# Performance work log

Hardware: AMD Instinct MI355X
Metric: run time of the kernel (lower is better)

The kernel has to match this reference:

```python
import jax, jax.numpy as jnp
import numpy as np

N_LEVELS = 8
N_FEATS = 8            # features per level
BASE_RES = 16
PER_LEVEL_SCALE = 1.2599210739135742
LOG2_HASHMAP = 19
TABLE_PAD = 8192       # padded per-level table rows (>= max level size 6568)
N_POINTS = 262144


def _level_params(l):
    # tcnn: scale = base * s^l - 1 ; res = ceil(scale)+1 ; size = min(2^19, round_up(res^2, 8))
    scale = BASE_RES * (PER_LEVEL_SCALE ** l) - 1.0
    res = int(np.ceil(scale)) + 1
    size = min(1 << LOG2_HASHMAP, ((res * res + 7) // 8) * 8)
    return float(scale), res, size


def hashgrid_encode(x, table):
    """x: [N,2] in [0,1), table: [L, TABLE_PAD, F]. Returns [N, L*F]."""
    outs = []
    for l in range(N_LEVELS):
        scale, res, size = _level_params(l)
        pos = x * jnp.float32(scale) + jnp.float32(0.5)
        pg = jnp.floor(pos)
        frac = pos - pg
        pg = pg.astype(jnp.int32)
        # Smoothstep interpolation weights: t^2 (3 - 2t)
        w = frac * frac * (3.0 - 2.0 * frac)          # [N,2]
        feat = jnp.zeros((x.shape[0], N_FEATS), dtype=table.dtype)
        for dx in (0, 1):
            wx = w[:, 0] if dx else 1.0 - w[:, 0]
            for dy in (0, 1):
                wy = w[:, 1] if dy else 1.0 - w[:, 1]
                # dense grid index (all levels here fit the hashmap), modulo level size as in tcnn
                idx = ((pg[:, 0] + dx) + (pg[:, 1] + dy) * res) % size
                feat = feat + (wx * wy)[:, None] * table[l, idx]  # irregular gather
        outs.append(feat)
    return jnp.concatenate(outs, axis=-1)  # [N, 64]


def mlp(enc, W0, W1, W2, W3):
    h = jax.nn.relu(enc @ W0)
    h = jax.nn.relu(h @ W1)
    h = jax.nn.relu(h @ W2)
    return h @ W3  # linear output activation


def setup_inputs() -> dict:
    key = jax.random.key(0)
    ks = jax.random.split(key, 6)
    x = jax.random.uniform(ks[0], (N_POINTS, 2), dtype=jnp.float32)
    # tcnn initializes grid params ~ uniform(-1e-4, 1e-4); small values
    table = jax.random.normal(ks[1], (N_LEVELS, TABLE_PAD, N_FEATS), dtype=jnp.float32) * 1e-2
    W0 = jax.random.normal(ks[2], (64, 256), dtype=jnp.float32) * (1.0 / np.sqrt(64))
    W1 = jax.random.normal(ks[3], (256, 256), dtype=jnp.float32) * (1.0 / np.sqrt(256))
    W2 = jax.random.normal(ks[4], (256, 256), dtype=jnp.float32) * (1.0 / np.sqrt(256))
    W3 = jax.random.normal(ks[5], (256, 1), dtype=jnp.float32) * (1.0 / np.sqrt(256))
    return {"x": x, "table": table, "W0": W0, "W1": W1, "W2": W2, "W3": W3}


def reference(x, table, W0, W1, W2, W3):
    enc = hashgrid_encode(x, table)
    return mlp(enc, W0, W1, W2, W3)  # [N, 1]
```

## Files before the change

### kernel.cpp

```cpp
#include <hip/hip_runtime.h>
#include <cmath>


#define N_LEVELS 8
#define TABLE_PAD 8192
#define TILE_M 64
#define ACT_STRIDE 264
#define ENC_STRIDE 72

typedef __attribute__((ext_vector_type(8))) short short8;
typedef __attribute__((ext_vector_type(16))) float float16v;

struct LevelParams {
  float scale[N_LEVELS];
  int   res[N_LEVELS];
  int   size[N_LEVELS];
};

__device__ __forceinline__ unsigned short f2bf(float f) {
  unsigned int u = __float_as_uint(f);
  u += 0x7fffu + ((u >> 16) & 1u);
  return (unsigned short)(u >> 16);
}
__device__ __forceinline__ unsigned int pack2bf(float a, float b) {
  a = a > 0.f ? a : 0.f;
  b = b > 0.f ? b : 0.f;
  return (unsigned int)f2bf(a) | ((unsigned int)f2bf(b) << 16);
}

__global__ void pack_weights_kernel(const float* __restrict__ W0,
                                    const float* __restrict__ W1,
                                    const float* __restrict__ W2,
                                    unsigned short* __restrict__ Wp) {
  int tid = blockIdx.x * blockDim.x + threadIdx.x;
  const float* src;
  int base, e;
  if (tid < 16384)        { src = W0; base = 0;     e = tid;         }
  else if (tid < 81920)   { src = W1; base = 16384; e = tid - 16384; }
  else if (tid < 147456)  { src = W2; base = 81920; e = tid - 81920; }
  else return;
  int ki = e & 15;
  int n  = (e >> 4) & 255;
  int kb = e >> 12;
  unsigned int u = __float_as_uint(src[(kb * 16 + ki) * 256 + n]);
  u += 0x7fffu + ((u >> 16) & 1u);
  Wp[base + e] = (unsigned short)(u >> 16);
}

__global__ __launch_bounds__(512, 6) void neural_field_kernel(
    const float* __restrict__ x,
    const float* __restrict__ table,
    const unsigned short* __restrict__ Wp,
    const float* __restrict__ W3,
    float* __restrict__ out,
    LevelParams P) {
  __shared__ unsigned short bufE[TILE_M * ENC_STRIDE];
  __shared__ unsigned short bufA[TILE_M * ACT_STRIDE];

  const int t  = threadIdx.x;
  const int g0 = blockIdx.x * TILE_M;

  const int lane  = t & 63;
  const int w     = t >> 6;
  const int l31   = lane & 31;
  const int h8    = lane >> 5;
  const int wbase = w * 32;

  const int woff = (wbase + l31) * 16 + h8 * 8;

  {
    int p = t & 63;
    int l = t >> 6;
    float2 xy = ((const float2*)x)[g0 + p];
    float scale = P.scale[l];
    int res = P.res[l], size = P.size[l];
    float posx = xy.x * scale + 0.5f;
    float posy = xy.y * scale + 0.5f;
    float pgx = floorf(posx), pgy = floorf(posy);
    float fx = posx - pgx, fy = posy - pgy;
    float wx = fx * fx * (3.0f - 2.0f * fx);
    float wy = fy * fy * (3.0f - 2.0f * fy);
    int px = (int)pgx, py = (int)pgy;
    float acc[8] = {0, 0, 0, 0, 0, 0, 0, 0};
    for (int dy = 0; dy < 2; ++dy) {
      float wyv = dy ? wy : 1.0f - wy;
      for (int dx = 0; dx < 2; ++dx) {
        float wgt = (dx ? wx : 1.0f - wx) * wyv;
        int idx = (px + dx) + (py + dy) * res;
        if (idx >= size) idx -= size;
        const float4* tp =
            (const float4*)(table + ((size_t)l * TABLE_PAD + idx) * 8);
        float4 t0 = tp[0], t1 = tp[1];
        acc[0] += wgt * t0.x; acc[1] += wgt * t0.y;
        acc[2] += wgt * t0.z; acc[3] += wgt * t0.w;
        acc[4] += wgt * t1.x; acc[5] += wgt * t1.y;
        acc[6] += wgt * t1.z; acc[7] += wgt * t1.w;
      }
    }
    union { unsigned short s[8]; short8 v; } u;
    for (int j = 0; j < 8; ++j) u.s[j] = f2bf(acc[j]);
    *(short8*)&bufE[p * ENC_STRIDE + l * 8] = u.v;
  }

  auto run_layer = [&](const unsigned short* inb, int in_stride,
                       unsigned short* outb, const unsigned short* Wpl,
                       int KB, short8 wf0, bool inplace, bool fuse_final,
                       float* fsum) {
    float16v acc[2];
    for (int j = 0; j < 16; ++j) { acc[0][j] = 0.f; acc[1][j] = 0.f; }

    const unsigned short* ap0 = &inb[l31 * in_stride + h8 * 8];
    const unsigned short* ap1 = ap0 + 32 * in_stride;
    const unsigned short* wp  = Wpl + woff;

    float w3f[16];
    if (fuse_final) {
      for (int q = 0; q < 4; ++q) {
        float4 wv = *(const float4*)(W3 + wbase + 8 * q + 4 * h8);
        w3f[4 * q + 0] = wv.x; w3f[4 * q + 1] = wv.y;
        w3f[4 * q + 2] = wv.z; w3f[4 * q + 3] = wv.w;
      }
    }

    short8 af0[2];
    af0[0] = *(const short8*)(ap0);
    af0[1] = *(const short8*)(ap1);

#pragma unroll
    for (int kb = 0; kb < KB; ++kb) {
      short8 wf1, af1[2];
      int kn = (kb + 1 < KB) ? kb + 1 : kb;
      wf1    = *(const short8*)(wp + kn * 4096);
      af1[0] = *(const short8*)(ap0 + kn * 16);
      af1[1] = *(const short8*)(ap1 + kn * 16);

      acc[0] = __builtin_amdgcn_mfma_f32_32x32x16_bf16(wf0, af0[0], acc[0],
                                                       0, 0, 0);
      acc[1] = __builtin_amdgcn_mfma_f32_32x32x16_bf16(wf0, af0[1], acc[1],
                                                       0, 0, 0);
      wf0 = wf1; af0[0] = af1[0]; af0[1] = af1[1];
    }

    if (inplace) __syncthreads();

    if (!fuse_final) {
      for (int pt = 0; pt < 2; ++pt) {
        int m = pt * 32 + l31;
        for (int q = 0; q < 4; ++q) {
          int n0 = wbase + 8 * q + 4 * h8;
          uint2 pk;
          pk.x = pack2bf(acc[pt][4 * q + 0], acc[pt][4 * q + 1]);
          pk.y = pack2bf(acc[pt][4 * q + 2], acc[pt][4 * q + 3]);
          *(uint2*)&outb[m * ACT_STRIDE + n0] = pk;
        }
      }
    } else {
      float part0 = 0.f, part1 = 0.f;
      for (int j = 0; j < 16; ++j) {
        float v0 = acc[0][j]; v0 = v0 > 0.f ? v0 : 0.f;
        float v1 = acc[1][j]; v1 = v1 > 0.f ? v1 : 0.f;
        part0 += v0 * w3f[j];
        part1 += v1 * w3f[j];
      }
      part0 += __shfl_xor(part0, 32);
      part1 += __shfl_xor(part1, 32);
      float val = h8 ? part1 : part0;
      fsum[lane * 9 + w] = val;
    }
  };

  float* fsum = (float*)bufE;

  short8 wf = *(const short8*)(Wp + woff);
  __syncthreads();
  run_layer(bufE, ENC_STRIDE, bufA, Wp, 4, wf, false, false, fsum);
  wf = *(const short8*)(Wp + 16384 + woff);
  __syncthreads();
  run_layer(bufA, ACT_STRIDE, bufA, Wp + 16384, 16, wf, true, false, fsum);
  wf = *(const short8*)(Wp + 81920 + woff);
  __syncthreads();
  run_layer(bufA, ACT_STRIDE, nullptr, Wp + 81920, 16, wf, false, true, fsum);
  __syncthreads();

  {
    int p = t >> 3;
    int q = t & 7;
    float v = fsum[p * 9 + q];
    v += __shfl_xor(v, 1);
    v += __shfl_xor(v, 2);
    v += __shfl_xor(v, 4);
    if (q == 0) out[g0 + p] = v;
  }
}

extern "C" void kernel_launch(void* const* d_in, const int* in_sizes, int n_in,
                              void* d_out, int out_size, void* d_ws,
                              size_t ws_size, hipStream_t stream) {
  const float* x     = (const float*)d_in[0];
  const float* table = (const float*)d_in[1];
  const float* W0    = (const float*)d_in[2];
  const float* W1    = (const float*)d_in[3];
  const float* W2    = (const float*)d_in[4];
  const float* W3    = (const float*)d_in[5];
  float* out = (float*)d_out;
  int N = in_sizes[0] / 2;

  unsigned short* Wp = (unsigned short*)d_ws;

  LevelParams P;
  const double c = 1.2599210739135742;
  double m = 1.0;
  for (int l = 0; l < N_LEVELS; ++l) {
    double scale_d = 16.0 * m - 1.0;
    int res = (int)std::ceil(scale_d) + 1;
    long long sz = ((long long)res * res + 7) / 8 * 8;
    if (sz > (1LL << 19)) sz = 1LL << 19;
    P.scale[l] = (float)scale_d;
    P.res[l]   = res;
    P.size[l]  = (int)sz;
    m *= c;
  }

  hipLaunchKernelGGL(pack_weights_kernel, dim3(576), dim3(256), 0, stream,
                     W0, W1, W2, Wp);
  hipLaunchKernelGGL(neural_field_kernel, dim3(N / TILE_M), dim3(512), 0,
                     stream, x, table, Wp, W3, out, P);
}
```

Before: 161.2 us.

## Double point tile to 128 and give each wave a 64x64 MFMA sub-tile

Raises the tile to 128 points per block and remaps the 8 waves into a 4x2 grid, where each wave computes 64 features by 64 points with four accumulators. Each loaded weight fragment is now reused across twice as many points, which halves weight traffic per point and cuts the final cross-wave reduction to 4 partials. The encoding is written straight into the shared activation buffer, so the separate encoding buffer goes away. In exchange shared memory per block doubles, the occupancy hint drops from 6 to 4, and register pressure rises with four accumulator tiles.

```diff
diff --git a/kernel.cpp b/kernel.cpp
--- a/kernel.cpp
+++ b/kernel.cpp
@@ -4,9 +4,8 @@
 
 #define N_LEVELS 8
 #define TABLE_PAD 8192
-#define TILE_M 64
+#define TILE_M 128
 #define ACT_STRIDE 264
-#define ENC_STRIDE 72
 
 typedef __attribute__((ext_vector_type(8))) short short8;
 typedef __attribute__((ext_vector_type(16))) float float16v;
@@ -47,15 +46,15 @@
   Wp[base + e] = (unsigned short)(u >> 16);
 }
 
-__global__ __launch_bounds__(512, 6) void neural_field_kernel(
+__global__ __launch_bounds__(512, 4) void neural_field_kernel(
     const float* __restrict__ x,
     const float* __restrict__ table,
     const unsigned short* __restrict__ Wp,
     const float* __restrict__ W3,
     float* __restrict__ out,
     LevelParams P) {
-  __shared__ unsigned short bufE[TILE_M * ENC_STRIDE];
   __shared__ unsigned short bufA[TILE_M * ACT_STRIDE];
+  __shared__ float fsum[TILE_M * 5];
 
   const int t  = threadIdx.x;
   const int g0 = blockIdx.x * TILE_M;
@@ -64,131 +63,142 @@
   const int w     = t >> 6;
   const int l31   = lane & 31;
   const int h8    = lane >> 5;
-  const int wbase = w * 32;
+  const int fg    = w & 3;
+  const int pg    = w >> 2;
+  const int wbase = fg * 64;
+  const int mbase = pg * 64;
 
   const int woff = (wbase + l31) * 16 + h8 * 8;
 
   {
-    int p = t & 63;
-    int l = t >> 6;
+    int p  = t & 127;
+    int lb = t >> 7;
     float2 xy = ((const float2*)x)[g0 + p];
-    float scale = P.scale[l];
-    int res = P.res[l], size = P.size[l];
-    float posx = xy.x * scale + 0.5f;
-    float posy = xy.y * scale + 0.5f;
-    float pgx = floorf(posx), pgy = floorf(posy);
-    float fx = posx - pgx, fy = posy - pgy;
-    float wx = fx * fx * (3.0f - 2.0f * fx);
-    float wy = fy * fy * (3.0f - 2.0f * fy);
-    int px = (int)pgx, py = (int)pgy;
-    float acc[8] = {0, 0, 0, 0, 0, 0, 0, 0};
-    for (int dy = 0; dy < 2; ++dy) {
-      float wyv = dy ? wy : 1.0f - wy;
-      for (int dx = 0; dx < 2; ++dx) {
-        float wgt = (dx ? wx : 1.0f - wx) * wyv;
-        int idx = (px + dx) + (py + dy) * res;
-        if (idx >= size) idx -= size;
-        const float4* tp =
-            (const float4*)(table + ((size_t)l * TABLE_PAD + idx) * 8);
-        float4 t0 = tp[0], t1 = tp[1];
-        acc[0] += wgt * t0.x; acc[1] += wgt * t0.y;
-        acc[2] += wgt * t0.z; acc[3] += wgt * t0.w;
-        acc[4] += wgt * t1.x; acc[5] += wgt * t1.y;
-        acc[6] += wgt * t1.z; acc[7] += wgt * t1.w;
+#pragma unroll
+    for (int li = 0; li < 2; ++li) {
+      int l = lb + li * 4;
+      float scale = P.scale[l];
+      int res = P.res[l], size = P.size[l];
+      float posx = xy.x * scale + 0.5f;
+      float posy = xy.y * scale + 0.5f;
+      float pgx = floorf(posx), pgy = floorf(posy);
+      float fx = posx - pgx, fy = posy - pgy;
+      float wxv = fx * fx * (3.0f - 2.0f * fx);
+      float wyv = fy * fy * (3.0f - 2.0f * fy);
+      int px = (int)pgx, py = (int)pgy;
+      float acc[8] = {0, 0, 0, 0, 0, 0, 0, 0};
+      for (int dy = 0; dy < 2; ++dy) {
+        float wy2 = dy ? wyv : 1.0f - wyv;
+        for (int dx = 0; dx < 2; ++dx) {
+          float wgt = (dx ? wxv : 1.0f - wxv) * wy2;
+          int idx = (px + dx) + (py + dy) * res;
+          if (idx >= size) idx -= size;
+          const float4* tp =
+              (const float4*)(table + ((size_t)l * TABLE_PAD + idx) * 8);
+          float4 t0 = tp[0], t1 = tp[1];
+          acc[0] += wgt * t0.x; acc[1] += wgt * t0.y;
+          acc[2] += wgt * t0.z; acc[3] += wgt * t0.w;
+          acc[4] += wgt * t1.x; acc[5] += wgt * t1.y;
+          acc[6] += wgt * t1.z; acc[7] += wgt * t1.w;
+        }
       }
-    }
-    union { unsigned short s[8]; short8 v; } u;
-    for (int j = 0; j < 8; ++j) u.s[j] = f2bf(acc[j]);
-    *(short8*)&bufE[p * ENC_STRIDE + l * 8] = u.v;
+      union { unsigned short s[8]; short8 v; } u;
+      for (int j = 0; j < 8; ++j) u.s[j] = f2bf(acc[j]);
+      *(short8*)&bufA[p * ACT_STRIDE + l * 8] = u.v;
+    }
   }
 
-  auto run_layer = [&](const unsigned short* inb, int in_stride,
-                       unsigned short* outb, const unsigned short* Wpl,
-                       int KB, short8 wf0, bool inplace, bool fuse_final,
-                       float* fsum) {
-    float16v acc[2];
-    for (int j = 0; j < 16; ++j) { acc[0][j] = 0.f; acc[1][j] = 0.f; }
-
-    const unsigned short* ap0 = &inb[l31 * in_stride + h8 * 8];
-    const unsigned short* ap1 = ap0 + 32 * in_stride;
+  auto run_layer = [&](const unsigned short* Wpl, int KB,
+                       short8 wfa, short8 wfb, bool fuse_final) {
+    float16v acc[2][2];
+#pragma unroll
+    for (int j = 0; j < 16; ++j) {
+      acc[0][0][j] = 0.f; acc[0][1][j] = 0.f;
+      acc[1][0][j] = 0.f; acc[1][1][j] = 0.f;
+    }
+
+    const unsigned short* ap0 = &bufA[(mbase + l31) * ACT_STRIDE + h8 * 8];
+    const unsigned short* ap1 = ap0 + 32 * ACT_STRIDE;
     const unsigned short* wp  = Wpl + woff;
 
-    float w3f[16];
-    if (fuse_final) {
-      for (int q = 0; q < 4; ++q) {
-        float4 wv = *(const float4*)(W3 + wbase + 8 * q + 4 * h8);
-        w3f[4 * q + 0] = wv.x; w3f[4 * q + 1] = wv.y;
-        w3f[4 * q + 2] = wv.z; w3f[4 * q + 3] = wv.w;
-      }
-    }
-
-    short8 af0[2];
-    af0[0] = *(const short8*)(ap0);
-    af0[1] = *(const short8*)(ap1);
-
 #pragma unroll
     for (int kb = 0; kb < KB; ++kb) {
-      short8 wf1, af1[2];
       int kn = (kb + 1 < KB) ? kb + 1 : kb;
-      wf1    = *(const short8*)(wp + kn * 4096);
-      af1[0] = *(const short8*)(ap0 + kn * 16);
-      af1[1] = *(const short8*)(ap1 + kn * 16);
-
-      acc[0] = __builtin_amdgcn_mfma_f32_32x32x16_bf16(wf0, af0[0], acc[0],
-                                                       0, 0, 0);
-      acc[1] = __builtin_amdgcn_mfma_f32_32x32x16_bf16(wf0, af0[1], acc[1],
-                                                       0, 0, 0);
-      wf0 = wf1; af0[0] = af1[0]; af0[1] = af1[1];
-    }
-
-    if (inplace) __syncthreads();
+      short8 wna = *(const short8*)(wp + kn * 4096);
+      short8 wnb = *(const short8*)(wp + kn * 4096 + 512);
+      short8 bf0 = *(const short8*)(ap0 + kb * 16);
+      short8 bf1 = *(const short8*)(ap1 + kb * 16);
+      acc[0][0] = __builtin_amdgcn_mfma_f32_32x32x16_bf16(wfa, bf0,
+                                                          acc[0][0], 0, 0, 0);
+      acc[0][1] = __builtin_amdgcn_mfma_f32_32x32x16_bf16(wfa, bf1,
+                                                          acc[0][1], 0, 0, 0);
+      acc[1][0] = __builtin_amdgcn_mfma_f32_32x32x16_bf16(wfb, bf0,
+                                                          acc[1][0], 0, 0, 0);
+      acc[1][1] = __builtin_amdgcn_mfma_f32_32x32x16_bf16(wfb, bf1,
+                                                          acc[1][1], 0, 0, 0);
+      wfa = wna; wfb = wnb;
+    }
 
     if (!fuse_final) {
-      for (int pt = 0; pt < 2; ++pt) {
-        int m = pt * 32 + l31;
-        for (int q = 0; q < 4; ++q) {
-          int n0 = wbase + 8 * q + 4 * h8;
-          uint2 pk;
-          pk.x = pack2bf(acc[pt][4 * q + 0], acc[pt][4 * q + 1]);
-          pk.y = pack2bf(acc[pt][4 * q + 2], acc[pt][4 * q + 3]);
-          *(uint2*)&outb[m * ACT_STRIDE + n0] = pk;
+      __syncthreads();
+#pragma unroll
+      for (int ft = 0; ft < 2; ++ft) {
+#pragma unroll
+        for (int pt = 0; pt < 2; ++pt) {
+          int m  = mbase + pt * 32 + l31;
+          int n0 = wbase + ft * 32 + 4 * h8;
+#pragma unroll
+          for (int q = 0; q < 4; ++q) {
+            uint2 pk;
+            pk.x = pack2bf(acc[ft][pt][4 * q + 0], acc[ft][pt][4 * q + 1]);
+            pk.y = pack2bf(acc[ft][pt][4 * q + 2], acc[ft][pt][4 * q + 3]);
+            *(uint2*)&bufA[m * ACT_STRIDE + n0 + 8 * q] = pk;
+          }
         }
       }
     } else {
       float part0 = 0.f, part1 = 0.f;
-      for (int j = 0; j < 16; ++j) {
-        float v0 = acc[0][j]; v0 = v0 > 0.f ? v0 : 0.f;
-        float v1 = acc[1][j]; v1 = v1 > 0.f ? v1 : 0.f;
-        part0 += v0 * w3f[j];
-        part1 += v1 * w3f[j];
+#pragma unroll
+      for (int ft = 0; ft < 2; ++ft) {
+#pragma unroll
+        for (int q = 0; q < 4; ++q) {
+          float4 wv = *(const float4*)(W3 + wbase + ft * 32 + 8 * q + 4 * h8);
+          float w3v[4] = {wv.x, wv.y, wv.z, wv.w};
+#pragma unroll
+          for (int r = 0; r < 4; ++r) {
+            float v0 = acc[ft][0][4 * q + r]; v0 = v0 > 0.f ? v0 : 0.f;
+            float v1 = acc[ft][1][4 * q + r]; v1 = v1 > 0.f ? v1 : 0.f;
+            part0 += v0 * w3v[r];
+            part1 += v1 * w3v[r];
+          }
+        }
       }
       part0 += __shfl_xor(part0, 32);
       part1 += __shfl_xor(part1, 32);
-      float val = h8 ? part1 : part0;
-      fsum[lane * 9 + w] = val;
+      fsum[(mbase + lane) * 5 + fg] = h8 ? part1 : part0;
     }
   };
 
-  float* fsum = (float*)bufE;
-
-  short8 wf = *(const short8*)(Wp + woff);
-  __syncthreads();
-  run_layer(bufE, ENC_STRIDE, bufA, Wp, 4, wf, false, false, fsum);
-  wf = *(const short8*)(Wp + 16384 + woff);
-  __syncthreads();
-  run_layer(bufA, ACT_STRIDE, bufA, Wp + 16384, 16, wf, true, false, fsum);
-  wf = *(const short8*)(Wp + 81920 + woff);
-  __syncthreads();
-  run_layer(bufA, ACT_STRIDE, nullptr, Wp + 81920, 16, wf, false, true, fsum);
+  short8 wfa = *(const short8*)(Wp + woff);
+  short8 wfb = *(const short8*)(Wp + woff + 512);
+  __syncthreads();
+  run_layer(Wp, 4, wfa, wfb, false);
+  wfa = *(const short8*)(Wp + 16384 + woff);
+  wfb = *(const short8*)(Wp + 16384 + woff + 512);
+  __syncthreads();
+  run_layer(Wp + 16384, 16, wfa, wfb, false);
+  wfa = *(const short8*)(Wp + 81920 + woff);
+  wfb = *(const short8*)(Wp + 81920 + woff + 512);
+  __syncthreads();
+  run_layer(Wp + 81920, 16, wfa, wfb, true);
   __syncthreads();
 
   {
-    int p = t >> 3;
-    int q = t & 7;
-    float v = fsum[p * 9 + q];
+    int p = t >> 2;
+    int q = t & 3;
+    float v = fsum[p * 5 + q];
     v += __shfl_xor(v, 1);
     v += __shfl_xor(v, 2);
-    v += __shfl_xor(v, 4);
     if (q == 0) out[g0 + p] = v;
   }
 }
```

After: 163.8 us. About the same (+1.6%).
